# Kernel tuning notes

Hardware: AMD Instinct MI355X
Metric: run time of the kernel (lower is better)

Reference implementation:

```python
import jax, jax.numpy as jnp
import numpy as np

N_NODES = 100_000
N_EDGES = 1_600_000
D = 128
BN_EPS = 1e-5
GIN_EPS = 0.0  # GINConv default eps, train_eps=False


def setup_inputs() -> dict:
    key = jax.random.key(0)
    ks = jax.random.split(key, 8)
    x = jax.random.normal(ks[0], (N_NODES, D), dtype=jnp.float32)
    edge_index = jax.random.randint(ks[1], (2, N_EDGES), 0, N_NODES, dtype=jnp.int64)
    s = 1.0 / np.sqrt(D)
    W1 = jax.random.uniform(ks[2], (D, D), jnp.float32, -s, s)
    b1 = jax.random.uniform(ks[3], (D,), jnp.float32, -s, s)
    W2 = jax.random.uniform(ks[4], (D, D), jnp.float32, -s, s)
    b2 = jax.random.uniform(ks[5], (D,), jnp.float32, -s, s)
    W3 = jax.random.uniform(ks[6], (D, D), jnp.float32, -s, s)
    g1 = jnp.ones((D,), jnp.float32)
    be1 = jnp.zeros((D,), jnp.float32)
    g2 = jnp.ones((D,), jnp.float32)
    be2 = jnp.zeros((D,), jnp.float32)
    return {"x": x, "edge_index": edge_index,
            "W1": W1, "b1": b1, "g1": g1, "be1": be1,
            "W2": W2, "b2": b2, "g2": g2, "be2": be2,
            "W3": W3}


def _batchnorm(h, gamma, beta):
    # training-mode BatchNorm1d over node dim with biased variance
    mean = jnp.mean(h, axis=0)
    var = jnp.mean(jnp.square(h - mean), axis=0)
    return (h - mean) * jax.lax.rsqrt(var + BN_EPS) * gamma + beta


def reference(x, edge_index, W1, b1, g1, be1, W2, b2, g2, be2, W3):
    src, dst = edge_index[0], edge_index[1]
    # GIN aggregation: (1+eps)*x_i + sum_{j->i} x_j  (scatter-add over edges)
    agg = jax.ops.segment_sum(x[src], dst, num_segments=N_NODES)
    h = (1.0 + GIN_EPS) * x + agg
    # MLP: Linear+BN+ReLU x2, then Linear (no bias)
    h = jax.nn.relu(_batchnorm(h @ W1.T + b1, g1, be1))
    h = jax.nn.relu(_batchnorm(h @ W2.T + b2, g2, be2))
    h = h @ W3.T
    # GINLayer final activation (bn=None)
    return jax.nn.relu(h)
```

## Files before the change

kernel.cpp:

```cpp
#include <hip/hip_runtime.h>

#define NN 100000
#define NE 1600000
#define DD 128
#define NCB 196
#define TILE 2048
#define NTILE 782
#define SREP 32
#define WPAD 17408
#define GROWS 256

typedef __attribute__((ext_vector_type(8))) short bf16x8;
typedef __attribute__((ext_vector_type(4))) float f32x4;

union u4bf8 { uint4 u; bf16x8 v; };

__device__ __forceinline__ ushort f2bf(float f) {
    union { float f; uint i; } v; v.f = f;
    uint i = v.i;
    return (ushort)((i + 0x7fffu + ((i >> 16) & 1u)) >> 16);
}
__device__ __forceinline__ float bf2f(ushort u) {
    union { uint i; float f; } v; v.i = ((uint)u) << 16; return v.f;
}
__device__ __forceinline__ float blo(uint v) { return bf2f((ushort)(v & 0xffffu)); }
__device__ __forceinline__ float bhi(uint v) { return bf2f((ushort)(v >> 16)); }

__global__ __launch_bounds__(256) void k_xbh(const float* __restrict__ x,
                                             uint* __restrict__ xb,
                                             const int* __restrict__ ei,
                                             int* __restrict__ ghistP,
                                             const float* __restrict__ W1,
                                             const float* __restrict__ W2,
                                             const float* __restrict__ W3,
                                             ushort* __restrict__ Wbp) {
    __shared__ int h[NCB];
    int t = threadIdx.x;
    if (t < NCB) h[t] = 0;
    __syncthreads();
    int base = blockIdx.x * TILE;
#pragma unroll
    for (int i = 0; i < 8; ++i) {
        int e = base + i * 256 + t;
        if (e < NE) atomicAdd(&h[ei[NE + e] >> 9], 1);
    }
    int gid = blockIdx.x * 256 + t;
#pragma unroll
    for (int i = 0; i < 8; ++i) {
        int item = i * (NTILE * 256) + gid;
        if (item < NN * 16) {
            int n = item >> 4, q = item & 15;
            const float* xp = x + (size_t)n * DD + q * 8;
            float4 a = *(const float4*)xp;
            float4 b = *(const float4*)(xp + 4);
            uint4 pk;
            pk.x = (uint)f2bf(a.x) | ((uint)f2bf(a.y) << 16);
            pk.y = (uint)f2bf(a.z) | ((uint)f2bf(a.w) << 16);
            pk.z = (uint)f2bf(b.x) | ((uint)f2bf(b.y) << 16);
            pk.w = (uint)f2bf(b.z) | ((uint)f2bf(b.w) << 16);
            *(uint4*)(xb + (size_t)n * 64 + q * 4) = pk;
        }
    }
    int c = gid;
    if (c < 6144) {
        int l = c >> 11;
        int cc = c & 2047;
        int r = cc >> 4, c8 = (cc & 15) * 8;
        const float* Wl = (l == 0) ? W1 : (l == 1) ? W2 : W3;
        const float* p = Wl + r * DD + c8;
        float4 a = *(const float4*)p;
        float4 b = *(const float4*)(p + 4);
        uint4 pk;
        pk.x = (uint)f2bf(a.x) | ((uint)f2bf(a.y) << 16);
        pk.y = (uint)f2bf(a.z) | ((uint)f2bf(a.w) << 16);
        pk.z = (uint)f2bf(b.x) | ((uint)f2bf(b.y) << 16);
        pk.w = (uint)f2bf(b.z) | ((uint)f2bf(b.w) << 16);
        *(uint4*)&Wbp[(size_t)l * WPAD + r * 136 + c8] = pk;
    }
    __syncthreads();
    if (t < NCB && h[t] > 0) atomicAdd(&ghistP[t * 16], h[t]);
}

__global__ void k_cscan(const int* __restrict__ ghistP, int* __restrict__ cb,
                        int* __restrict__ gcurP) {
    __shared__ int sh[256];
    int t = threadIdx.x;
    int my = (t < NCB) ? ghistP[t * 16] : 0;
    sh[t] = my;
    __syncthreads();
    for (int o = 1; o < 256; o <<= 1) {
        int u = (t >= o) ? sh[t - o] : 0;
        __syncthreads();
        sh[t] += u;
        __syncthreads();
    }
    if (t < NCB) { int ex = sh[t] - my; cb[t] = ex; gcurP[t * 16] = ex; }
    if (t == NCB - 1) cb[NCB] = sh[t];
}

__global__ __launch_bounds__(256) void k_cscatter(const int* __restrict__ ei,
                                                  int* __restrict__ gcurP,
                                                  uint* __restrict__ buck) {
    __shared__ int h[NCB];
    __shared__ int tb[NCB];
    int t = threadIdx.x;
    if (t < NCB) h[t] = 0;
    __syncthreads();
    int base = blockIdx.x * TILE;
    uint vv[8]; int bb[8], rr[8];
#pragma unroll
    for (int i = 0; i < 8; ++i) {
        int e = base + i * 256 + t;
        bb[i] = -1;
        if (e < NE) {
            int s = ei[e], d = ei[NE + e];
            int b = d >> 9;
            bb[i] = b;
            vv[i] = (uint)s | ((uint)(d & 511) << 17);
            rr[i] = atomicAdd(&h[b], 1);
        }
    }
    __syncthreads();
    if (t < NCB && h[t] > 0) tb[t] = atomicAdd(&gcurP[t * 16], h[t]);
    __syncthreads();
#pragma unroll
    for (int i = 0; i < 8; ++i) {
        if (bb[i] >= 0) buck[tb[bb[i]] + rr[i]] = vv[i];
    }
}

__global__ __launch_bounds__(256) void k_fsort(const uint* __restrict__ buck,
                                               const int* __restrict__ cb,
                                               int* __restrict__ csr,
                                               int* __restrict__ rowp) {
    __shared__ int cnt[512];
    __shared__ int sd[256];
    int c = blockIdx.x, t = threadIdx.x;
    cnt[t] = 0; cnt[t + 256] = 0;
    __syncthreads();
    int s0 = cb[c], s1 = cb[c + 1];
    for (int i = s0 + t; i < s1; i += 256)
        atomicAdd(&cnt[(buck[i] >> 17) & 511], 1);
    __syncthreads();
    int p = cnt[2 * t], q = cnt[2 * t + 1];
    sd[t] = p + q;
    __syncthreads();
    for (int o = 1; o < 256; o <<= 1) {
        int u = (t >= o) ? sd[t - o] : 0;
        __syncthreads();
        sd[t] += u;
        __syncthreads();
    }
    int base = sd[t] - (p + q);
    rowp[c * 512 + 2 * t]     = s0 + base;
    rowp[c * 512 + 2 * t + 1] = s0 + base + p;
    __syncthreads();
    cnt[2 * t] = base;
    cnt[2 * t + 1] = base + p;
    __syncthreads();
    for (int i = s0 + t; i < s1; i += 256) {
        uint v = buck[i];
        int ld = (int)((v >> 17) & 511u);
        int pos = atomicAdd(&cnt[ld], 1);
        csr[s0 + pos] = (int)(v & 0x1FFFFu);
    }
}

#define B8(ACC0, ACC1, SJ, J)                                               \
    {                                                                       \
        int s0 = __shfl(SJ, J),     s1 = __shfl(SJ, J + 1);                 \
        int s2 = __shfl(SJ, J + 2), s3 = __shfl(SJ, J + 3);                 \
        int s4 = __shfl(SJ, J + 4), s5 = __shfl(SJ, J + 5);                 \
        int s6 = __shfl(SJ, J + 6), s7 = __shfl(SJ, J + 7);                 \
        uint v0 = xb[(size_t)s0 * 64 + lane], v1 = xb[(size_t)s1 * 64 + lane]; \
        uint v2 = xb[(size_t)s2 * 64 + lane], v3 = xb[(size_t)s3 * 64 + lane]; \
        uint v4 = xb[(size_t)s4 * 64 + lane], v5 = xb[(size_t)s5 * 64 + lane]; \
        uint v6 = xb[(size_t)s6 * 64 + lane], v7 = xb[(size_t)s7 * 64 + lane]; \
        ACC0 += blo(v0) + blo(v1) + blo(v2) + blo(v3)                       \
              + blo(v4) + blo(v5) + blo(v6) + blo(v7);                      \
        ACC1 += bhi(v0) + bhi(v1) + bhi(v2) + bhi(v3)                       \
              + bhi(v4) + bhi(v5) + bhi(v6) + bhi(v7);                      \
    }

__global__ __launch_bounds__(256) void k_gather(const uint* __restrict__ xb,
                                                const int* __restrict__ rowp,
                                                const int* __restrict__ csr,
                                                ushort* __restrict__ agg) {
    const int HALF = NN / 2;
    int wave = threadIdx.x >> 6, lane = threadIdx.x & 63;
    int w = blockIdx.x * 4 + wave;
    if (w >= HALF) return;
    int nA = w, nB = w + HALF;
    uint sA = xb[(size_t)nA * 64 + lane];
    uint sB = xb[(size_t)nB * 64 + lane];
    float a0 = blo(sA), a1 = bhi(sA);
    float b0 = blo(sB), b1 = bhi(sB);
    int iA = rowp[nA], eA = rowp[nA + 1];
    int iB = rowp[nB], eB = rowp[nB + 1];

    while (iA < eA || iB < eB) {
        int mA = eA - iA; if (mA > 64) mA = 64; if (mA < 0) mA = 0;
        int mB = eB - iB; if (mB > 64) mB = 64; if (mB < 0) mB = 0;
        int sjA = (lane < mA) ? csr[iA + lane] : 0;
        int sjB = (lane < mB) ? csr[iB + lane] : 0;
        int j = 0, k = 0;
        while (j + 8 <= mA && k + 8 <= mB) {
            int t0 = __shfl(sjA, j),     t1 = __shfl(sjA, j + 1);
            int t2 = __shfl(sjA, j + 2), t3 = __shfl(sjA, j + 3);
            int t4 = __shfl(sjA, j + 4), t5 = __shfl(sjA, j + 5);
            int t6 = __shfl(sjA, j + 6), t7 = __shfl(sjA, j + 7);
            int u0 = __shfl(sjB, k),     u1 = __shfl(sjB, k + 1);
            int u2 = __shfl(sjB, k + 2), u3 = __shfl(sjB, k + 3);
            int u4 = __shfl(sjB, k + 4), u5 = __shfl(sjB, k + 5);
            int u6 = __shfl(sjB, k + 6), u7 = __shfl(sjB, k + 7);
            uint vA0 = xb[(size_t)t0 * 64 + lane], vA1 = xb[(size_t)t1 * 64 + lane];
            uint vA2 = xb[(size_t)t2 * 64 + lane], vA3 = xb[(size_t)t3 * 64 + lane];
            uint vA4 = xb[(size_t)t4 * 64 + lane], vA5 = xb[(size_t)t5 * 64 + lane];
            uint vA6 = xb[(size_t)t6 * 64 + lane], vA7 = xb[(size_t)t7 * 64 + lane];
            uint vB0 = xb[(size_t)u0 * 64 + lane], vB1 = xb[(size_t)u1 * 64 + lane];
            uint vB2 = xb[(size_t)u2 * 64 + lane], vB3 = xb[(size_t)u3 * 64 + lane];
            uint vB4 = xb[(size_t)u4 * 64 + lane], vB5 = xb[(size_t)u5 * 64 + lane];
            uint vB6 = xb[(size_t)u6 * 64 + lane], vB7 = xb[(size_t)u7 * 64 + lane];
            a0 += blo(vA0) + blo(vA1) + blo(vA2) + blo(vA3)
                + blo(vA4) + blo(vA5) + blo(vA6) + blo(vA7);
            a1 += bhi(vA0) + bhi(vA1) + bhi(vA2) + bhi(vA3)
                + bhi(vA4) + bhi(vA5) + bhi(vA6) + bhi(vA7);
            b0 += blo(vB0) + blo(vB1) + blo(vB2) + blo(vB3)
                + blo(vB4) + blo(vB5) + blo(vB6) + blo(vB7);
            b1 += bhi(vB0) + bhi(vB1) + bhi(vB2) + bhi(vB3)
                + bhi(vB4) + bhi(vB5) + bhi(vB6) + bhi(vB7);
            j += 8; k += 8;
        }
        while (j + 8 <= mA) { B8(a0, a1, sjA, j) j += 8; }
        while (k + 8 <= mB) { B8(b0, b1, sjB, k) k += 8; }
        while (j < mA && k < mB) {
            int t = __shfl(sjA, j); int u = __shfl(sjB, k);
            uint vA = xb[(size_t)t * 64 + lane];
            uint vB = xb[(size_t)u * 64 + lane];
            a0 += blo(vA); a1 += bhi(vA);
            b0 += blo(vB); b1 += bhi(vB);
            ++j; ++k;
        }
        while (j < mA) {
            int t = __shfl(sjA, j++);
            uint vA = xb[(size_t)t * 64 + lane];
            a0 += blo(vA); a1 += bhi(vA);
        }
        while (k < mB) {
            int u = __shfl(sjB, k++);
            uint vB = xb[(size_t)u * 64 + lane];
            b0 += blo(vB); b1 += bhi(vB);
        }
        iA += mA; iB += mB;
    }

    uint pkA = (uint)f2bf(a0) | ((uint)f2bf(a1) << 16);
    uint pkB = (uint)f2bf(b0) | ((uint)f2bf(b1) << 16);
    ((uint*)(agg + (size_t)nA * DD))[lane] = pkA;
    ((uint*)(agg + (size_t)nB * DD))[lane] = pkB;
}

template <int MODE>
__global__ __launch_bounds__(256) void k_gemm(const ushort* __restrict__ Ain,
                                              const ushort* __restrict__ Wp,
                                              const float* __restrict__ bias,
                                              const float* __restrict__ statsIn,
                                              const float* __restrict__ g,
                                              const float* __restrict__ be,
                                              void* __restrict__ Outv,
                                              float* __restrict__ statsOut) {
    __shared__ __align__(16) ushort lw[DD * 136];
    __shared__ float red[2][4][DD];
    __shared__ float lac[2 * DD];

    int tid = threadIdx.x;
#pragma unroll
    for (int it = 0; it < 8; ++it) {
        int o8 = (it * 256 + tid) * 8;
        *(uint4*)&lw[o8] = *(const uint4*)&Wp[o8];
    }
    if (tid < 128) {
        int o8 = 16384 + tid * 8;
        *(uint4*)&lw[o8] = *(const uint4*)&Wp[o8];
    }
    if constexpr (MODE != 1) {
        if (tid < DD) {
            float S = 0.f, Q = 0.f;
#pragma unroll
            for (int r = 0; r < SREP; ++r) {
                S += statsIn[(r << 8) + tid];
                Q += statsIn[(r << 8) + DD + tid];
            }
            float inv = 1.f / (float)NN;
            float mean = S * inv;
            float var = Q * inv - mean * mean;
            float a = g[tid] * rsqrtf(var + 1e-5f);
            lac[tid] = a;
            lac[DD + tid] = be[tid] - mean * a;
        }
    }
    __syncthreads();

    int wave = tid >> 6, lane = tid & 63;
    int lm = lane & 15, quad = lane >> 4;
    ushort* Out16 = (ushort*)Outv;
    float* Out32 = (float*)Outv;

    float csum[8], csq[8];
#pragma unroll
    for (int nt = 0; nt < 8; ++nt) { csum[nt] = 0.f; csq[nt] = 0.f; }

#pragma unroll
    for (int sub = 0; sub < 4; ++sub) {
        int row0 = blockIdx.x * GROWS + sub * 64 + wave * 16;
        int arow = row0 + lm;
        int ar = (arow < NN) ? arow : 0;

        bf16x8 afrag[4];
#pragma unroll
        for (int kb = 0; kb < 4; ++kb) {
            int k0 = kb * 32 + quad * 8;
            const ushort* ap = Ain + (size_t)ar * DD + k0;
            u4bf8 u; u.u = *(const uint4*)ap;
            if constexpr (MODE == 1) {
                afrag[kb] = u.v;
            } else {
                uint pk[4] = {u.u.x, u.u.y, u.u.z, u.u.w};
                bf16x8 af;
#pragma unroll
                for (int jj = 0; jj < 4; ++jj) {
                    int k = k0 + jj * 2;
                    float v0 = blo(pk[jj]);
                    float v1 = bhi(pk[jj]);
                    v0 = fmaxf(fmaf(v0, lac[k], lac[DD + k]), 0.f);
                    v1 = fmaxf(fmaf(v1, lac[k + 1], lac[DD + k + 1]), 0.f);
                    af[jj * 2]     = (short)f2bf(v0);
                    af[jj * 2 + 1] = (short)f2bf(v1);
                }
                afrag[kb] = af;
            }
        }

        f32x4 acc[8];
#pragma unroll
        for (int nt = 0; nt < 8; ++nt) {
            float bv = (MODE == 3) ? 0.f : bias[nt * 16 + lm];
            acc[nt] = (f32x4){bv, bv, bv, bv};
        }

#pragma unroll
        for (int kb = 0; kb < 4; ++kb) {
#pragma unroll
            for (int nt = 0; nt < 8; ++nt) {
                bf16x8 bfrag = *(const bf16x8*)&lw[(nt * 16 + lm) * 136 + kb * 32 + quad * 8];
                acc[nt] = __builtin_amdgcn_mfma_f32_16x16x32_bf16(afrag[kb], bfrag, acc[nt], 0, 0, 0);
            }
        }

#pragma unroll
        for (int nt = 0; nt < 8; ++nt) {
            int col = nt * 16 + lm;
#pragma unroll
            for (int r = 0; r < 4; ++r) {
                int row = row0 + quad * 4 + r;
                float v = acc[nt][r];
                if (MODE == 3) v = fmaxf(v, 0.f);
                if (row < NN) {
                    if constexpr (MODE == 3) Out32[(size_t)row * DD + col] = v;
                    else Out16[(size_t)row * DD + col] = f2bf(v);
                    csum[nt] += v;
                    csq[nt] += v * v;
                }
            }
        }
    }

    if constexpr (MODE != 3) {
#pragma unroll
        for (int nt = 0; nt < 8; ++nt) {
            float s = csum[nt], q = csq[nt];
            s += __shfl_down(s, 16, 64); q += __shfl_down(q, 16, 64);
            s += __shfl_down(s, 32, 64); q += __shfl_down(q, 32, 64);
            if (quad == 0) {
                red[0][wave][nt * 16 + lm] = s;
                red[1][wave][nt * 16 + lm] = q;
            }
        }
        __syncthreads();
        if (tid < DD) {
            float S = red[0][0][tid] + red[0][1][tid] + red[0][2][tid] + red[0][3][tid];
            float Q = red[1][0][tid] + red[1][1][tid] + red[1][2][tid] + red[1][3][tid];
            int rep = (blockIdx.x & (SREP - 1)) << 8;
            atomicAdd(&statsOut[rep + tid], S);
            atomicAdd(&statsOut[rep + DD + tid], Q);
        }
    }
}

extern "C" void kernel_launch(void* const* d_in, const int* in_sizes, int n_in,
                              void* d_out, int out_size, void* d_ws, size_t ws_size,
                              hipStream_t stream) {
    const float* x   = (const float*)d_in[0];
    const int* ei    = (const int*)d_in[1];
    const float* W1  = (const float*)d_in[2];
    const float* b1  = (const float*)d_in[3];
    const float* g1  = (const float*)d_in[4];
    const float* be1 = (const float*)d_in[5];
    const float* W2  = (const float*)d_in[6];
    const float* b2  = (const float*)d_in[7];
    const float* g2  = (const float*)d_in[8];
    const float* be2 = (const float*)d_in[9];
    const float* W3  = (const float*)d_in[10];

    float* stats  = (float*)d_ws;
    float* stats2 = stats + SREP * 256;
    int* ghistP   = (int*)(stats2 + SREP * 256);
    ushort* Wbp   = (ushort*)(ghistP + NCB * 16);
    int* cb       = (int*)(Wbp + 3 * WPAD);
    int* gcurP    = cb + NCB + 4;
    int* rowp     = gcurP + NCB * 16;
    uint* buck    = (uint*)(rowp + NCB * 512 + 4);
    int* csr      = (int*)(buck + NE);
    ushort* agg   = (ushort*)(((uintptr_t)(csr + NE) + 15) & ~(uintptr_t)15);
    uint* xb     = (uint*)d_out;
    ushort* t1   = (ushort*)d_out + (size_t)NN * DD;
    ushort* t2   = agg;
    float* outp  = (float*)d_out;

    int gblk = (NN + GROWS - 1) / GROWS;
    hipMemsetAsync(stats, 0, (2 * SREP * 256) * sizeof(float) + NCB * 16 * sizeof(int), stream);
    k_xbh<<<NTILE, 256, 0, stream>>>(x, xb, ei, ghistP, W1, W2, W3, Wbp);
    k_cscan<<<1, 256, 0, stream>>>(ghistP, cb, gcurP);
    k_cscatter<<<NTILE, 256, 0, stream>>>(ei, gcurP, buck);
    k_fsort<<<NCB, 256, 0, stream>>>(buck, cb, csr, rowp);
    k_gather<<<(NN / 2 + 3) / 4, 256, 0, stream>>>(xb, rowp, csr, agg);
    k_gemm<1><<<gblk, 256, 0, stream>>>(agg, Wbp, b1, nullptr, nullptr, nullptr, t1, stats);
    k_gemm<2><<<gblk, 256, 0, stream>>>(t1, Wbp + WPAD, b2, stats, g1, be1, t2, stats2);
    k_gemm<3><<<gblk, 256, 0, stream>>>(t2, Wbp + 2 * WPAD, nullptr, stats2, g2, be2, outp, nullptr);
}
```

Before: 303.3 us.

## Fuse bucket scan into scatter and sort kernels, cache buckets in LDS

Removes the single-block k_cscan launch: k_cscatter and k_fsort each recompute the exclusive prefix over the bucket histogram in shared memory, and gcurP now holds relative offsets zeroed by the memset. Scatter tiles double to 4096 edges, halving block count and global atomics. k_fsort stages its bucket into a 48KB LDS buffer so the second pass does not reread global memory. The GEMM kernels prefetch the first A-fragment before loading weights. In exchange every block redoes a 256-wide scan, and the large LDS buffer may lower occupancy.

```diff
diff --git a/kernel.cpp b/kernel.cpp
--- a/kernel.cpp
+++ b/kernel.cpp
@@ -6,6 +6,9 @@
 #define NCB 196
 #define TILE 2048
 #define NTILE 782
+#define TILEC 4096
+#define NTILEC 391
+#define FCAP 12288
 #define SREP 32
 #define WPAD 17408
 #define GROWS 256
@@ -81,35 +84,20 @@
     if (t < NCB && h[t] > 0) atomicAdd(&ghistP[t * 16], h[t]);
 }
 
-__global__ void k_cscan(const int* __restrict__ ghistP, int* __restrict__ cb,
-                        int* __restrict__ gcurP) {
-    __shared__ int sh[256];
-    int t = threadIdx.x;
-    int my = (t < NCB) ? ghistP[t * 16] : 0;
-    sh[t] = my;
-    __syncthreads();
-    for (int o = 1; o < 256; o <<= 1) {
-        int u = (t >= o) ? sh[t - o] : 0;
-        __syncthreads();
-        sh[t] += u;
-        __syncthreads();
-    }
-    if (t < NCB) { int ex = sh[t] - my; cb[t] = ex; gcurP[t * 16] = ex; }
-    if (t == NCB - 1) cb[NCB] = sh[t];
-}
-
 __global__ __launch_bounds__(256) void k_cscatter(const int* __restrict__ ei,
+                                                  const int* __restrict__ ghistP,
                                                   int* __restrict__ gcurP,
                                                   uint* __restrict__ buck) {
     __shared__ int h[NCB];
     __shared__ int tb[NCB];
+    __shared__ int sh[256];
     int t = threadIdx.x;
     if (t < NCB) h[t] = 0;
     __syncthreads();
-    int base = blockIdx.x * TILE;
-    uint vv[8]; int bb[8], rr[8];
-#pragma unroll
-    for (int i = 0; i < 8; ++i) {
+    int base = blockIdx.x * TILEC;
+    uint vv[16]; int bb[16]; int rr[16];
+#pragma unroll
+    for (int i = 0; i < 16; ++i) {
         int e = base + i * 256 + t;
         bb[i] = -1;
         if (e < NE) {
@@ -121,26 +109,54 @@
         }
     }
     __syncthreads();
-    if (t < NCB && h[t] > 0) tb[t] = atomicAdd(&gcurP[t * 16], h[t]);
-    __syncthreads();
-#pragma unroll
-    for (int i = 0; i < 8; ++i) {
+    int my = (t < NCB) ? ghistP[t * 16] : 0;
+    sh[t] = my;
+    __syncthreads();
+    for (int o = 1; o < 256; o <<= 1) {
+        int u = (t >= o) ? sh[t - o] : 0;
+        __syncthreads();
+        sh[t] += u;
+        __syncthreads();
+    }
+    if (t < NCB && h[t] > 0)
+        tb[t] = (sh[t] - my) + atomicAdd(&gcurP[t * 16], h[t]);
+    __syncthreads();
+#pragma unroll
+    for (int i = 0; i < 16; ++i) {
         if (bb[i] >= 0) buck[tb[bb[i]] + rr[i]] = vv[i];
     }
 }
 
 __global__ __launch_bounds__(256) void k_fsort(const uint* __restrict__ buck,
-                                               const int* __restrict__ cb,
+                                               const int* __restrict__ ghistP,
                                                int* __restrict__ csr,
                                                int* __restrict__ rowp) {
+    __shared__ uint ebuf[FCAP];
     __shared__ int cnt[512];
     __shared__ int sd[256];
+    __shared__ int sh[256];
     int c = blockIdx.x, t = threadIdx.x;
     cnt[t] = 0; cnt[t + 256] = 0;
-    __syncthreads();
-    int s0 = cb[c], s1 = cb[c + 1];
-    for (int i = s0 + t; i < s1; i += 256)
-        atomicAdd(&cnt[(buck[i] >> 17) & 511], 1);
+    int my = (t < NCB) ? ghistP[t * 16] : 0;
+    sh[t] = my;
+    __syncthreads();
+    for (int o = 1; o < 256; o <<= 1) {
+        int u = (t >= o) ? sh[t - o] : 0;
+        __syncthreads();
+        sh[t] += u;
+        __syncthreads();
+    }
+    int s1 = sh[c];
+    int hc = ghistP[c * 16];
+    int s0 = s1 - hc;
+    int len = hc;
+    int cap = (len < FCAP) ? len : FCAP;
+    for (int i = t; i < cap; i += 256) ebuf[i] = buck[s0 + i];
+    __syncthreads();
+    for (int i = t; i < len; i += 256) {
+        uint v = (i < FCAP) ? ebuf[i] : buck[s0 + i];
+        atomicAdd(&cnt[(v >> 17) & 511], 1);
+    }
     __syncthreads();
     int p = cnt[2 * t], q = cnt[2 * t + 1];
     sd[t] = p + q;
@@ -158,8 +174,8 @@
     cnt[2 * t] = base;
     cnt[2 * t + 1] = base + p;
     __syncthreads();
-    for (int i = s0 + t; i < s1; i += 256) {
-        uint v = buck[i];
+    for (int i = t; i < len; i += 256) {
+        uint v = (i < FCAP) ? ebuf[i] : buck[s0 + i];
         int ld = (int)((v >> 17) & 511u);
         int pos = atomicAdd(&cnt[ld], 1);
         csr[s0 + pos] = (int)(v & 0x1FFFFu);
@@ -274,6 +290,17 @@
     __shared__ float lac[2 * DD];
 
     int tid = threadIdx.x;
+    int wave = tid >> 6, lane = tid & 63;
+    int lm = lane & 15, quad = lane >> 4;
+
+    int row00 = blockIdx.x * GROWS + wave * 16;
+    int ar0 = (row00 + lm < NN) ? row00 + lm : 0;
+    uint4 araw[4];
+#pragma unroll
+    for (int kb = 0; kb < 4; ++kb) {
+        araw[kb] = *(const uint4*)(Ain + (size_t)ar0 * DD + kb * 32 + quad * 8);
+    }
+
 #pragma unroll
     for (int it = 0; it < 8; ++it) {
         int o8 = (it * 256 + tid) * 8;
@@ -301,8 +328,6 @@
     }
     __syncthreads();
 
-    int wave = tid >> 6, lane = tid & 63;
-    int lm = lane & 15, quad = lane >> 4;
     ushort* Out16 = (ushort*)Outv;
     float* Out32 = (float*)Outv;
 
@@ -320,8 +345,9 @@
 #pragma unroll
         for (int kb = 0; kb < 4; ++kb) {
             int k0 = kb * 32 + quad * 8;
-            const ushort* ap = Ain + (size_t)ar * DD + k0;
-            u4bf8 u; u.u = *(const uint4*)ap;
+            u4bf8 u;
+            if (sub == 0) u.u = araw[kb];
+            else          u.u = *(const uint4*)(Ain + (size_t)ar * DD + k0);
             if constexpr (MODE == 1) {
                 afrag[kb] = u.v;
             } else {
@@ -415,10 +441,9 @@
     float* stats  = (float*)d_ws;
     float* stats2 = stats + SREP * 256;
     int* ghistP   = (int*)(stats2 + SREP * 256);
-    ushort* Wbp   = (ushort*)(ghistP + NCB * 16);
-    int* cb       = (int*)(Wbp + 3 * WPAD);
-    int* gcurP    = cb + NCB + 4;
-    int* rowp     = gcurP + NCB * 16;
+    int* gcurP    = ghistP + NCB * 16;
+    ushort* Wbp   = (ushort*)(gcurP + NCB * 16);
+    int* rowp     = (int*)(Wbp + 3 * WPAD);
     uint* buck    = (uint*)(rowp + NCB * 512 + 4);
     int* csr      = (int*)(buck + NE);
     ushort* agg   = (ushort*)(((uintptr_t)(csr + NE) + 15) & ~(uintptr_t)15);
@@ -428,11 +453,10 @@
     float* outp  = (float*)d_out;
 
     int gblk = (NN + GROWS - 1) / GROWS;
-    hipMemsetAsync(stats, 0, (2 * SREP * 256) * sizeof(float) + NCB * 16 * sizeof(int), stream);
+    hipMemsetAsync(stats, 0, (2 * SREP * 256) * sizeof(float) + 2 * NCB * 16 * sizeof(int), stream);
     k_xbh<<<NTILE, 256, 0, stream>>>(x, xb, ei, ghistP, W1, W2, W3, Wbp);
-    k_cscan<<<1, 256, 0, stream>>>(ghistP, cb, gcurP);
-    k_cscatter<<<NTILE, 256, 0, stream>>>(ei, gcurP, buck);
-    k_fsort<<<NCB, 256, 0, stream>>>(buck, cb, csr, rowp);
+    k_cscatter<<<NTILEC, 256, 0, stream>>>(ei, ghistP, gcurP, buck);
+    k_fsort<<<NCB, 256, 0, stream>>>(buck, ghistP, csr, rowp);
     k_gather<<<(NN / 2 + 3) / 4, 256, 0, stream>>>(xb, rowp, csr, agg);
     k_gemm<1><<<gblk, 256, 0, stream>>>(agg, Wbp, b1, nullptr, nullptr, nullptr, t1, stats);
     k_gemm<2><<<gblk, 256, 0, stream>>>(t1, Wbp + WPAD, b2, stats, g1, be1, t2, stats2);
```

Measured after the change: 292.9 us, median of 2. 1.04x faster.
